# Kernel optimization log

Measured on AMD Instinct MI355X. Metric: run time of the kernel, lower is better.

## Reference

```python
import jax, jax.numpy as jnp
import numpy as np

B, CDD, HIS, S, D, NH, FF, V, K = 8, 5, 50, 64, 768, 12, 3072, 30522, 8


def _ln(x):
    mu = x.mean(-1, keepdims=True)
    var = ((x - mu) ** 2).mean(-1, keepdims=True)
    return (x - mu) / jnp.sqrt(var + 1e-12)


def _transformer(x, mask, Wq, Wk, Wv, Wo, W1, W2):
    # x: [..., S, D]; mask: [..., S] (float, >0 means valid)
    lead = x.shape[:-2]
    s, d = x.shape[-2], x.shape[-1]
    dh = d // NH
    x2 = x.reshape(-1, s, d)
    m = mask.reshape(-1, s)
    split = lambda t: t.reshape(-1, s, NH, dh).transpose(0, 2, 1, 3)
    q, k, v = split(x2 @ Wq), split(x2 @ Wk), split(x2 @ Wv)
    logits = jnp.einsum('nhqd,nhkd->nhqk', q, k) / jnp.sqrt(jnp.float32(dh))
    logits = logits + jnp.where(m > 0, 0.0, -1e9)[:, None, None, :]
    a = jax.nn.softmax(logits, axis=-1)
    o = jnp.einsum('nhqk,nhkd->nhqd', a, v).transpose(0, 2, 1, 3).reshape(-1, s, d) @ Wo
    h = _ln(x2 + o)
    h = _ln(h + jax.nn.gelu(h @ W1) @ W2)
    h = h.reshape(*lead, s, d)
    return h, h[..., 0, :]


def _build_prefix(subword_index, mask):
    # subword_index: [B, n, S, 2] int; mask: [B, n, 1] float
    b, n = subword_index.shape[0], subword_index.shape[1]
    flat = subword_index[..., 0] * S + subword_index[..., 1]  # [B, n, S]
    dest = jnp.zeros((b * n, S * S), jnp.float32)
    dest = dest.at[jnp.arange(b * n)[:, None], flat.reshape(b * n, S)].set(1.0)
    dest = dest * mask.reshape(b * n, 1)
    prefix = dest.reshape(b, n, S, S)
    # granularity == 'avg' -> L1 normalize rows
    prefix = prefix / jnp.maximum(prefix.sum(-1, keepdims=True), 1e-12)
    return prefix


def setup_inputs() -> dict:
    key = jax.random.key(0)
    ks = jax.random.split(key, 24)
    w = lambda k, shp: jax.random.normal(k, shp, jnp.float32) * 0.02
    inp = {
        'cdd_subword_index': jax.random.randint(ks[0], (B, CDD, S, 2), 0, S, jnp.int32),
        'his_subword_index': jax.random.randint(ks[1], (B, HIS, S, 2), 0, S, jnp.int32),
        'cdd_encoded_index': jax.random.randint(ks[2], (B, CDD, S), 0, V, jnp.int32),
        'his_encoded_index': jax.random.randint(ks[3], (B, HIS, S), 0, V, jnp.int32),
        'cdd_mask': jnp.ones((B, CDD, 1), jnp.float32),
        'his_mask': jnp.ones((B, HIS, 1), jnp.float32),
        'cdd_attn_mask': jnp.ones((B, CDD, S), jnp.float32),
        'his_attn_mask': jnp.ones((B, HIS, S), jnp.float32),
        'emb': w(ks[4], (V, D)),
        'bert_Wq': w(ks[5], (D, D)), 'bert_Wk': w(ks[6], (D, D)),
        'bert_Wv': w(ks[7], (D, D)), 'bert_Wo': w(ks[8], (D, D)),
        'bert_W1': w(ks[9], (D, FF)), 'bert_W2': w(ks[10], (FF, D)),
        'encN_Wq': w(ks[11], (D, D)), 'encN_Wk': w(ks[12], (D, D)),
        'encN_Wv': w(ks[13], (D, D)), 'encN_Wo': w(ks[14], (D, D)),
        'encN_W1': w(ks[15], (D, FF)), 'encN_W2': w(ks[16], (FF, D)),
        'qU': w(ks[17], (D,)),
        'proj_W': w(ks[18], (D, D)), 'proj_b': jnp.zeros((D,), jnp.float32),
    }
    return inp


def reference(cdd_subword_index, his_subword_index, cdd_encoded_index, his_encoded_index,
              cdd_mask, his_mask, cdd_attn_mask, his_attn_mask, emb,
              bert_Wq, bert_Wk, bert_Wv, bert_Wo, bert_W1, bert_W2,
              encN_Wq, encN_Wk, encN_Wv, encN_Wo, encN_W1, encN_W2,
              qU, proj_W, proj_b):
    rt_d = jnp.sqrt(jnp.float32(D))
    # scatter-built one-hot subword->token prefix matrices
    cdd_prefix = _build_prefix(cdd_subword_index, cdd_mask)   # [B,C,S,S]
    his_prefix = _build_prefix(his_subword_index, his_mask)   # [B,H,S,S]
    # pooled attention masks: prefix @ mask
    cdd_attn = jnp.einsum('bcst,bct->bcs', cdd_prefix, cdd_attn_mask)
    his_attn = jnp.einsum('bnst,bnt->bns', his_prefix, his_attn_mask)
    # embedding lookup + subword->token pooling
    cdd_emb = jnp.einsum('bcst,bctd->bcsd', cdd_prefix, emb[cdd_encoded_index])
    his_emb = jnp.einsum('bnst,bntd->bnsd', his_prefix, emb[his_encoded_index])
    # candidate news: BERT encode, take CLS, project
    _, cdd_cls = _transformer(cdd_emb, cdd_attn, bert_Wq, bert_Wk, bert_Wv, bert_Wo, bert_W1, bert_W2)
    cdd_repr = jnp.tanh(cdd_cls @ proj_W + proj_b)            # [B,C,D]
    # history news encoder
    his_hidden, his_cls = _transformer(his_emb, his_attn, encN_Wq, encN_Wk, encN_Wv, encN_Wo, encN_W1, encN_W2)
    # user encoder: attention pooling over history news reprs
    wgt = jax.nn.softmax(jnp.einsum('bnd,d->bn', his_cls, qU) / rt_d, axis=-1)
    user0 = jnp.einsum('bn,bnd->bd', wgt, his_cls)            # [B,D]
    # matching reducer: top-k personalized terms per history news
    scores = jnp.einsum('bnsd,bd->bns', his_hidden, user0) / rt_d
    scores = jnp.where(his_attn > 0, scores, -1e9)
    _, kid = jax.lax.top_k(scores, K)                         # [B,H,K]
    ps_terms = jnp.take_along_axis(his_hidden, kid[..., None], axis=2).reshape(B, HIS * K, D)
    ps_mask = jnp.take_along_axis(his_attn, kid, axis=2).reshape(B, HIS * K)
    # user BERT over selected terms
    _, user_cls = _transformer(ps_terms, ps_mask, bert_Wq, bert_Wk, bert_Wv, bert_Wo, bert_W1, bert_W2)
    user_repr = jnp.tanh(user_cls @ proj_W + proj_b)          # [B,D]
    score = jnp.einsum('bcd,bd->bc', cdd_repr, user_repr) / rt_d
    prob = jax.nn.log_softmax(score, axis=1)
    return prob, kid
```

## Files before the change

kernel.cpp:

```cpp
#include <hip/hip_runtime.h>
#include <math.h>

#define DIM 768
#define NHEAD 12
#define DHEAD 64
#define FFDIM 3072

typedef _Float16 v8h __attribute__((ext_vector_type(8)));
typedef float v4f __attribute__((ext_vector_type(4)));

__device__ __forceinline__ float gelu_f(float x) {
    float x3 = x * x * x;
    return 0.5f * x * (1.0f + tanhf(0.7978845608028654f * (x + 0.044715f * x3)));
}

__device__ __forceinline__ void gl_lds16(const _Float16* g, _Float16* l) {
    __builtin_amdgcn_global_load_lds(
        (const __attribute__((address_space(1))) unsigned int*)(g),
        (__attribute__((address_space(3))) unsigned int*)(l),
        16, 0, 0);
}

struct GemmP {
    const _Float16* A1; const _Float16* A2;
    const _Float16* eB1[3]; const _Float16* eB2[3]; const _Float16* bB1[3];
    float* C[3];
    _Float16* G1; _Float16* G2;
    int bnd;
};

__global__ __launch_bounds__(256) void gemm_mfma(GemmP p, int M, int N, int K,
                                                 int epi, float cdiv, float gscale, int nbg)
{
    __shared__ _Float16 sm[2][4][128 * 32];
    const int tid = threadIdx.x;
    const int w = tid >> 6, lane = tid & 63;
    const int lm = lane & 15, kg = lane >> 4;

    const int nb = (int)gridDim.x, mb = (int)gridDim.y;
    const int nwg = nb * mb * (int)gridDim.z;
    int lid = (int)blockIdx.x + nb * ((int)blockIdx.y + mb * (int)blockIdx.z);
    int qd = nwg >> 3, rm = nwg & 7;
    int xcd = lid & 7, pos = lid >> 3;
    int wid = (xcd < rm ? xcd * (qd + 1) : rm * (qd + 1) + (xcd - rm) * qd) + pos;
    int gsz = (nbg > 0 && (nb % nbg) == 0) ? nbg : 1;
    int ngrp = nb / gsz;
    int bxi = wid % gsz; int tt = wid / gsz;
    int by = tt % mb; tt /= mb;
    int bxg = tt % ngrp;
    int z = tt / ngrp;
    const int row0 = by << 7, col0 = (bxg * gsz + bxi) << 7;

    const int wm = (w >> 1) << 6, wn = (w & 1) << 6;
    const int rl = (w << 4) + (lane >> 2);
    const int cofs = (lane & 3) << 3;
    int nt; const _Float16 *B1p, *B2p;
    if (row0 < p.bnd) { nt = 3; B1p = p.eB1[z]; B2p = p.eB2[z]; }
    else             { nt = 1; B1p = p.bB1[z]; B2p = p.bB1[z]; }
    const _Float16* A1 = p.A1 + (size_t)row0 * K;
    const _Float16* A2 = p.A2 + (size_t)row0 * K;
    const _Float16* B1 = B1p + (size_t)col0 * K;
    const _Float16* B2 = B2p + (size_t)col0 * K;
    const int ldsLo = w * 512, ldsHi = (w + 4) * 512;
    const size_t gbase = (size_t)rl * K + cofs;

    v4f acc[4][4];
#pragma unroll
    for (int i = 0; i < 4; i++)
#pragma unroll
        for (int j = 0; j < 4; j++) acc[i][j] = (v4f){0.f, 0.f, 0.f, 0.f};

    auto stage = [&](int d, int k0) {
        size_t glo = gbase + k0;
        size_t ghi = glo + (size_t)64 * K;
        gl_lds16(A1 + glo, sm[d][0] + ldsLo); gl_lds16(A1 + ghi, sm[d][0] + ldsHi);
        gl_lds16(B1 + glo, sm[d][2] + ldsLo); gl_lds16(B1 + ghi, sm[d][2] + ldsHi);
        if (nt == 3) {
            gl_lds16(A2 + glo, sm[d][1] + ldsLo); gl_lds16(A2 + ghi, sm[d][1] + ldsHi);
            gl_lds16(B2 + glo, sm[d][3] + ldsLo); gl_lds16(B2 + ghi, sm[d][3] + ldsHi);
        }
    };

    const int nk = K >> 5;
    stage(0, 0);
    __syncthreads();
    for (int i = 0; i < nk; i++) {
        int cur = i & 1;
        if (i + 1 < nk) stage(cur ^ 1, (i + 1) << 5);
        const _Float16* sA1 = sm[cur][0]; const _Float16* sA2 = sm[cur][1];
        const _Float16* sB1 = sm[cur][2]; const _Float16* sB2 = sm[cur][3];
        v8h a1[4], b1f[4];
#pragma unroll
        for (int i2 = 0; i2 < 4; i2++) {
            a1[i2]  = *(const v8h*)(sA1 + (wm + (i2 << 4) + lm) * 32 + (kg << 3));
            b1f[i2] = *(const v8h*)(sB1 + (wn + (i2 << 4) + lm) * 32 + (kg << 3));
        }
        if (nt == 3) {
            v8h a2[4], b2f[4];
#pragma unroll
            for (int i2 = 0; i2 < 4; i2++) {
                a2[i2]  = *(const v8h*)(sA2 + (wm + (i2 << 4) + lm) * 32 + (kg << 3));
                b2f[i2] = *(const v8h*)(sB2 + (wn + (i2 << 4) + lm) * 32 + (kg << 3));
            }
#pragma unroll
            for (int i2 = 0; i2 < 4; i2++)
#pragma unroll
                for (int j = 0; j < 4; j++) {
                    acc[i2][j] = __builtin_amdgcn_mfma_f32_16x16x32_f16(a1[i2], b1f[j], acc[i2][j], 0, 0, 0);
                    acc[i2][j] = __builtin_amdgcn_mfma_f32_16x16x32_f16(a1[i2], b2f[j], acc[i2][j], 0, 0, 0);
                    acc[i2][j] = __builtin_amdgcn_mfma_f32_16x16x32_f16(a2[i2], b1f[j], acc[i2][j], 0, 0, 0);
                }
        } else {
#pragma unroll
            for (int i2 = 0; i2 < 4; i2++)
#pragma unroll
                for (int j = 0; j < 4; j++)
                    acc[i2][j] = __builtin_amdgcn_mfma_f32_16x16x32_f16(a1[i2], b1f[j], acc[i2][j], 0, 0, 0);
        }
        __syncthreads();
    }
    float* C = p.C[z];
#pragma unroll
    for (int i = 0; i < 4; i++) {
        int rb = row0 + wm + (i << 4) + (kg << 2);
#pragma unroll
        for (int j = 0; j < 4; j++) {
            int cc = col0 + wn + (j << 4) + lm;
#pragma unroll
            for (int r = 0; r < 4; r++) {
                float c = acc[i][j][r] * cdiv;
                size_t idx = (size_t)(rb + r) * N + cc;
                if (epi == 0) {
                    C[idx] = c;
                } else {
                    float gv = gelu_f(c) * gscale;
                    _Float16 g1 = (_Float16)gv;
                    p.G1[idx] = g1;
                    p.G2[idx] = (_Float16)(gv - (float)g1);
                }
            }
        }
    }
}

struct WJobs {
    const float* src[12];
    _Float16* d1[12]; _Float16* d2[12];
    int K[12]; int N[12]; int start[12];
};
__global__ __launch_bounds__(256) void wsplit_tr(WJobs jb)
{
    __shared__ float sh[32 * 33];
    int bid = blockIdx.x;
    int ji = 0;
#pragma unroll
    for (int i = 1; i < 12; i++) if (bid >= jb.start[i]) ji = i;
    const float* src = jb.src[ji];
    _Float16* d1 = jb.d1[ji]; _Float16* d2 = jb.d2[ji];
    int K = jb.K[ji], N = jb.N[ji];
    int t = bid - jb.start[ji];
    int tilesN = N >> 5;
    int tk = t / tilesN, tn = t - tk * tilesN;
    int k0 = tk << 5, n0 = tn << 5;
    int c = threadIdx.x & 31, rr = threadIdx.x >> 5;
#pragma unroll
    for (int pph = 0; pph < 4; pph++) {
        int r = rr + (pph << 3);
        sh[c * 33 + r] = src[(size_t)(k0 + r) * N + n0 + c];
    }
    __syncthreads();
#pragma unroll
    for (int pph = 0; pph < 4; pph++) {
        int rn = rr + (pph << 3);
        float v = sh[rn * 33 + c] * 64.f;
        _Float16 b1 = (_Float16)v;
        size_t idx = (size_t)(n0 + rn) * K + k0 + c;
        d1[idx] = b1;
        if (d2) d2[idx] = (_Float16)(v - (float)b1);
    }
}

__global__ __launch_bounds__(256) void build_prefix2(const int* __restrict__ hisSub,
    const float* __restrict__ hisMask, const float* __restrict__ hisAmask,
    const int* __restrict__ cddSub, const float* __restrict__ cddMask,
    const float* __restrict__ cddAmask,
    float* __restrict__ P, float* __restrict__ hisA, float* __restrict__ cddA)
{
    __shared__ float pref[64 * 64];
    int g = blockIdx.x;
    const int* sub; const float* mask; const float* amask; float* aout; int li;
    if (g < 400) { sub = hisSub; mask = hisMask; amask = hisAmask; aout = hisA; li = g; }
    else         { sub = cddSub; mask = cddMask; amask = cddAmask; aout = cddA; li = g - 400; }
    int tid = threadIdx.x;
    for (int t = tid; t < 4096; t += 256) pref[t] = 0.f;
    __syncthreads();
    if (tid < 64) {
        int r = sub[((size_t)li * 64 + tid) * 2 + 0];
        int c = sub[((size_t)li * 64 + tid) * 2 + 1];
        pref[(r << 6) + c] = 1.0f;
    }
    __syncthreads();
    float m = mask[li];
    int lane = tid & 63, w = tid >> 6;
    for (int s = (w << 4); s < (w << 4) + 16; s++) {
        float v = pref[(s << 6) + lane] * m;
        float rs = v;
#pragma unroll
        for (int o = 32; o; o >>= 1) rs += __shfl_down(rs, o);
        rs = __shfl(rs, 0);
        float nv = v / fmaxf(rs, 1e-12f);
        P[(((size_t)g << 6) + s) * 64 + lane] = nv;
        float av = nv * amask[((size_t)li << 6) + lane];
#pragma unroll
        for (int o = 32; o; o >>= 1) av += __shfl_down(av, o);
        if (lane == 0) aout[((size_t)li << 6) + s] = av;
    }
}

__global__ __launch_bounds__(256) void emb_pool2(const float* __restrict__ P,
    const int* __restrict__ encHis, const int* __restrict__ encCdd,
    const float* __restrict__ emb, float* __restrict__ X,
    _Float16* __restrict__ s1, _Float16* __restrict__ s2, int gOffHis, int gMid)
{
    int gl = blockIdx.x >> 2, q = blockIdx.x & 3;
    int g; const int* enc;
    if (gl < gMid) { g = gOffHis + gl; enc = encHis + (size_t)g * 64; }
    else { int gc = gl - gMid; g = 400 + gc; enc = encCdd + (size_t)gc * 64; }
    int tid = threadIdx.x;
    __shared__ float pw[16][64];
    __shared__ int tk[64];
    if (tid < 64) tk[tid] = enc[tid];
    for (int u = tid; u < 1024; u += 256) {
        int si = u >> 6, t = u & 63;
        pw[si][t] = P[((size_t)g * 64 + q * 16 + si) * 64 + t];
    }
    __syncthreads();
    float acc[16][3];
#pragma unroll
    for (int si = 0; si < 16; si++) { acc[si][0] = 0.f; acc[si][1] = 0.f; acc[si][2] = 0.f; }
    for (int t = 0; t < 64; t++) {
        const float* er = emb + (size_t)tk[t] * DIM;
        float e0 = er[tid], e1 = er[tid + 256], e2 = er[tid + 512];
#pragma unroll
        for (int si = 0; si < 16; si++) {
            float w = pw[si][t];
            acc[si][0] = fmaf(w, e0, acc[si][0]);
            acc[si][1] = fmaf(w, e1, acc[si][1]);
            acc[si][2] = fmaf(w, e2, acc[si][2]);
        }
    }
#pragma unroll
    for (int si = 0; si < 16; si++) {
        size_t base = ((size_t)gl * 64 + q * 16 + si) * DIM;
#pragma unroll
        for (int cci = 0; cci < 3; cci++) {
            int cc = tid + (cci << 8);
            float v = acc[si][cci];
            X[base + cc] = v;
            float xs = v * 64.f;
            _Float16 a = (_Float16)xs;
            s1[base + cc] = a;
            s2[base + cc] = (_Float16)(xs - (float)a);
        }
    }
}

__global__ __launch_bounds__(256) void attn_fused64(const float* __restrict__ Q,
    const float* __restrict__ Km, const float* __restrict__ V,
    const float* __restrict__ maskHis, const float* __restrict__ maskCdd, int gMid,
    _Float16* __restrict__ o1, _Float16* __restrict__ o2)
{
    __shared__ float Ks[64 * 65];
    __shared__ float Vs[64 * 65];
    __shared__ float Qs[64 * 65];
    int h = blockIdx.x % NHEAD;
    int g = blockIdx.x / NHEAD;
    const float* mrow = (g < gMid) ? maskHis + (size_t)g * 64
                                   : maskCdd + (size_t)(g - gMid) * 64;
    int tid = threadIdx.x, lane = tid & 63, w = tid >> 6;
    {
        int r = tid >> 2, c0 = (tid & 3) << 4;
        const float* qp = Q  + ((size_t)g * 64 + r) * DIM + h * DHEAD + c0;
        const float* kp = Km + ((size_t)g * 64 + r) * DIM + h * DHEAD + c0;
        const float* vp = V  + ((size_t)g * 64 + r) * DIM + h * DHEAD + c0;
#pragma unroll
        for (int u = 0; u < 16; u += 4) {
            float4 qv = *(const float4*)(qp + u);
            float4 kv = *(const float4*)(kp + u);
            float4 vv = *(const float4*)(vp + u);
            int o = r * 65 + c0 + u;
            Qs[o+0]=qv.x; Qs[o+1]=qv.y; Qs[o+2]=qv.z; Qs[o+3]=qv.w;
            Ks[o+0]=kv.x; Ks[o+1]=kv.y; Ks[o+2]=kv.z; Ks[o+3]=kv.w;
            Vs[o+0]=vv.x; Vs[o+1]=vv.y; Vs[o+2]=vv.z; Vs[o+3]=vv.w;
        }
    }
    __syncthreads();
    float mk = mrow[lane] > 0.f ? 0.f : -1e9f;
    for (int il = 0; il < 16; il++) {
        int i = (w << 4) + il;
        float d = 0.f;
        for (int t = 0; t < 64; t++) d = fmaf(Qs[i * 65 + t], Ks[lane * 65 + t], d);
        float l = d * 0.125f + mk;
        float mx = l;
#pragma unroll
        for (int o = 32; o; o >>= 1) mx = fmaxf(mx, __shfl_xor(mx, o));
        float e = expf(l - mx);
        float s = e;
#pragma unroll
        for (int o = 32; o; o >>= 1) s += __shfl_xor(s, o);
        float p = e / s;
        float acc = 0.f;
        for (int j = 0; j < 64; j++) {
            float pj = __shfl(p, j);
            acc = fmaf(pj, Vs[j * 65 + lane], acc);
        }
        size_t ob = ((size_t)g * 64 + i) * DIM + h * DHEAD + lane;
        float os = acc * 64.f;
        _Float16 h1 = (_Float16)os;
        o1[ob] = h1;
        o2[ob] = (_Float16)(os - (float)h1);
    }
}

#define SSTR 449
__global__ __launch_bounds__(256) void attn_flash400(const float* __restrict__ Q,
    const float* __restrict__ Km, const float* __restrict__ V,
    const float* __restrict__ mask, _Float16* __restrict__ o1, _Float16* __restrict__ o2)
{
    __shared__ _Float16 Kt[64 * 64];
    __shared__ float Sc[16 * SSTR];
    int qt = blockIdx.x % 25;
    int h  = (blockIdx.x / 25) % NHEAD;
    int g  = blockIdx.x / (25 * NHEAD);
    int tid = threadIdx.x, w = tid >> 6, lane = tid & 63, lm = lane & 15, kg = lane >> 4;

    v8h aq0, aq1;
    {
        const float* qp = Q + ((size_t)(g * 400 + qt * 16 + lm)) * DIM + h * DHEAD;
#pragma unroll
        for (int u = 0; u < 8; u++) {
            aq0[u] = (_Float16)qp[kg * 8 + u];
            aq1[u] = (_Float16)qp[32 + kg * 8 + u];
        }
    }
    for (int jt = 0; jt < 7; jt++) {
        int j0 = jt * 64;
        __syncthreads();
        {
            int jr = tid >> 2, c0 = (tid & 3) << 4;
            int j = j0 + jr;
            _Float16* kd = Kt + jr * 64 + c0;
            if (j < 400) {
                const float* kp = Km + ((size_t)(g * 400 + j)) * DIM + h * DHEAD + c0;
#pragma unroll
                for (int u = 0; u < 16; u++) kd[u] = (_Float16)kp[u];
            } else {
#pragma unroll
                for (int u = 0; u < 16; u++) kd[u] = (_Float16)0.f;
            }
        }
        __syncthreads();
        v8h b0, b1;
#pragma unroll
        for (int u = 0; u < 8; u++) {
            b0[u] = Kt[(w * 16 + lm) * 64 + kg * 8 + u];
            b1[u] = Kt[(w * 16 + lm) * 64 + 32 + kg * 8 + u];
        }
        v4f c = {0.f, 0.f, 0.f, 0.f};
        c = __builtin_amdgcn_mfma_f32_16x16x32_f16(aq0, b0, c, 0, 0, 0);
        c = __builtin_amdgcn_mfma_f32_16x16x32_f16(aq1, b1, c, 0, 0, 0);
        int jj = j0 + w * 16 + lm;
        float mv = (jj < 400) ? (mask[g * 400 + jj] > 0.f ? 0.f : -1e9f) : -1e9f;
#pragma unroll
        for (int r = 0; r < 4; r++)
            Sc[(kg * 4 + r) * SSTR + jj] = c[r] * 0.125f + mv;
    }
    __syncthreads();
    for (int rr = 0; rr < 4; rr++) {
        int r = w * 4 + rr;
        float mx = -INFINITY;
#pragma unroll
        for (int c7 = 0; c7 < 7; c7++) mx = fmaxf(mx, Sc[r * SSTR + c7 * 64 + lane]);
#pragma unroll
        for (int o = 32; o; o >>= 1) mx = fmaxf(mx, __shfl_xor(mx, o));
        float s = 0.f;
        float ev[7];
#pragma unroll
        for (int c7 = 0; c7 < 7; c7++) { ev[c7] = expf(Sc[r * SSTR + c7 * 64 + lane] - mx); s += ev[c7]; }
#pragma unroll
        for (int o = 32; o; o >>= 1) s += __shfl_xor(s, o);
        float inv = 1.f / s;
#pragma unroll
        for (int c7 = 0; c7 < 7; c7++) Sc[r * SSTR + c7 * 64 + lane] = ev[c7] * inv;
    }
    __syncthreads();
    v4f o = {0.f, 0.f, 0.f, 0.f};
    for (int kc = 0; kc < 14; kc++) {
        v8h a, b;
#pragma unroll
        for (int u = 0; u < 8; u++) a[u] = (_Float16)Sc[lm * SSTR + kc * 32 + kg * 8 + u];
#pragma unroll
        for (int u = 0; u < 8; u++) {
            int j = kc * 32 + kg * 8 + u;
            b[u] = (j < 400) ? (_Float16)V[((size_t)(g * 400 + j)) * DIM + h * DHEAD + w * 16 + lm]
                             : (_Float16)0.f;
        }
        o = __builtin_amdgcn_mfma_f32_16x16x32_f16(a, b, o, 0, 0, 0);
    }
#pragma unroll
    for (int r = 0; r < 4; r++) {
        int qr = qt * 16 + kg * 4 + r;
        size_t ob = ((size_t)(g * 400 + qr)) * DIM + h * DHEAD + w * 16 + lm;
        float os = o[r] * 64.f;
        _Float16 h1 = (_Float16)os;
        o1[ob] = h1; o2[ob] = (_Float16)(os - (float)h1);
    }
}

__global__ __launch_bounds__(256) void add_ln2(const float* __restrict__ X,
    const float* __restrict__ Y, float* __restrict__ outA, float* __restrict__ outB,
    int bndRow, _Float16* __restrict__ S1, _Float16* __restrict__ S2, float ss,
    float* __restrict__ cls, int clsOffA, int clsOffB, int S)
{
    int r = blockIdx.x, tid = threadIdx.x;
    size_t base = (size_t)r * DIM;
    float v0 = X[base + tid] + Y[base + tid];
    float v1 = X[base + tid + 256] + Y[base + tid + 256];
    float v2 = X[base + tid + 512] + Y[base + tid + 512];
    __shared__ float red[256];
    red[tid] = v0 + v1 + v2; __syncthreads();
    for (int o = 128; o; o >>= 1) { if (tid < o) red[tid] += red[tid + o]; __syncthreads(); }
    float mu = red[0] * (1.f / 768.f);
    __syncthreads();
    float d0 = v0 - mu, d1 = v1 - mu, d2 = v2 - mu;
    red[tid] = d0 * d0 + d1 * d1 + d2 * d2; __syncthreads();
    for (int o = 128; o; o >>= 1) { if (tid < o) red[tid] += red[tid + o]; __syncthreads(); }
    float rstd = rsqrtf(red[0] * (1.f / 768.f) + 1e-12f);
    float o0 = d0 * rstd, o1 = d1 * rstd, o2 = d2 * rstd;
    float* Out = (r < bndRow) ? outA + base : outB + (size_t)(r - bndRow) * DIM;
    Out[tid] = o0; Out[tid + 256] = o1; Out[tid + 512] = o2;
    if (S1) {
        float x0 = o0 * ss, x1 = o1 * ss, x2 = o2 * ss;
        _Float16 a0 = (_Float16)x0, a1 = (_Float16)x1, a2 = (_Float16)x2;
        S1[base + tid] = a0;        S2[base + tid] = (_Float16)(x0 - (float)a0);
        S1[base + tid + 256] = a1;  S2[base + tid + 256] = (_Float16)(x1 - (float)a1);
        S1[base + tid + 512] = a2;  S2[base + tid + 512] = (_Float16)(x2 - (float)a2);
    }
    if (cls && (r % S) == 0) {
        int g = (r < bndRow) ? clsOffA + r / S : clsOffB + (r - bndRow) / S;
        float* cd = cls + (size_t)g * DIM;
        cd[tid] = o0; cd[tid + 256] = o1; cd[tid + 512] = o2;
    }
}

__global__ __launch_bounds__(256) void gemm_kernel(const float* __restrict__ A,
    const float* __restrict__ B, float* __restrict__ C,
    int M, int N, int Kd, int epi, const float* __restrict__ bias)
{
    __shared__ float As[16][64];
    __shared__ float Bs[16][64];
    int tid = threadIdx.x;
    int tx = tid & 15, ty = tid >> 4;
    int row0 = blockIdx.y << 6, col0 = blockIdx.x << 6;
    int ar = tid >> 2, ak = (tid & 3) << 2;
    int bc = tid & 63, bk0 = tid >> 6;
    const float* Ap = A + (size_t)(row0 + ar) * Kd + ak;
    const float* Bp = B + (size_t)bk0 * N + col0 + bc;
    bool aval = (row0 + ar) < M;
    float acc[4][4];
#pragma unroll
    for (int i = 0; i < 4; i++)
#pragma unroll
        for (int j = 0; j < 4; j++) acc[i][j] = 0.f;
    for (int k0 = 0; k0 < Kd; k0 += 16) {
        float4 a4 = make_float4(0.f, 0.f, 0.f, 0.f);
        if (aval) a4 = *(const float4*)(Ap + k0);
        As[ak + 0][ar] = a4.x; As[ak + 1][ar] = a4.y;
        As[ak + 2][ar] = a4.z; As[ak + 3][ar] = a4.w;
#pragma unroll
        for (int i = 0; i < 4; i++)
            Bs[bk0 + 4 * i][bc] = Bp[(size_t)(k0 + 4 * i) * N];
        __syncthreads();
#pragma unroll
        for (int kk = 0; kk < 16; kk++) {
            float4 av = *(const float4*)&As[kk][ty << 2];
            float4 bv = *(const float4*)&Bs[kk][tx << 2];
            float aa[4] = {av.x, av.y, av.z, av.w};
            float bb[4] = {bv.x, bv.y, bv.z, bv.w};
#pragma unroll
            for (int i = 0; i < 4; i++)
#pragma unroll
                for (int j = 0; j < 4; j++)
                    acc[i][j] = fmaf(aa[i], bb[j], acc[i][j]);
        }
        __syncthreads();
    }
#pragma unroll
    for (int i = 0; i < 4; i++) {
        int r = row0 + (ty << 2) + i;
        if (r >= M) continue;
        float v[4];
#pragma unroll
        for (int j = 0; j < 4; j++) {
            float x = acc[i][j];
            if (epi == 1) x = gelu_f(x);
            else if (epi == 2) x = tanhf(x + bias[col0 + (tx << 2) + j]);
            v[j] = x;
        }
        *(float4*)(C + (size_t)r * N + col0 + (tx << 2)) = make_float4(v[0], v[1], v[2], v[3]);
    }
}

__global__ __launch_bounds__(256) void user_pool_kernel(const float* __restrict__ cls,
    const float* __restrict__ qU, float* __restrict__ user0)
{
    int b = blockIdx.x, tid = threadIdx.x;
    __shared__ float red[256];
    __shared__ float wv[64];
    const float scale = 0.03608439182435161f;
    for (int n = 0; n < 50; n++) {
        const float* cr = cls + ((size_t)(b * 50 + n)) * DIM;
        float d = 0.f;
        for (int t = tid; t < DIM; t += 256) d = fmaf(cr[t], qU[t], d);
        red[tid] = d; __syncthreads();
        for (int o = 128; o; o >>= 1) { if (tid < o) red[tid] += red[tid + o]; __syncthreads(); }
        if (tid == 0) wv[n] = red[0] * scale;
        __syncthreads();
    }
    if (tid == 0) {
        float mx = -INFINITY;
        for (int n = 0; n < 50; n++) mx = fmaxf(mx, wv[n]);
        float s = 0.f;
        for (int n = 0; n < 50; n++) { float e = expf(wv[n] - mx); wv[n] = e; s += e; }
        float inv = 1.f / s;
        for (int n = 0; n < 50; n++) wv[n] *= inv;
    }
    __syncthreads();
    for (int d = tid; d < DIM; d += 256) {
        float a = 0.f;
        for (int n = 0; n < 50; n++) a = fmaf(wv[n], cls[((size_t)(b * 50 + n)) * DIM + d], a);
        user0[(size_t)b * DIM + d] = a;
    }
}

__global__ __launch_bounds__(256) void topk_kernel(const float* __restrict__ hid,
    const float* __restrict__ user0, const float* __restrict__ attn,
    float* __restrict__ kid_f, int* __restrict__ kid_i, float* __restrict__ ps_mask)
{
    int bn = blockIdx.x;
    int b = bn / 50;
    int tid = threadIdx.x, lane = tid & 63, w = tid >> 6;
    __shared__ float sc[64];
    const float* u = user0 + (size_t)b * DIM;
    const float scale = 0.03608439182435161f;
    for (int s = w; s < 64; s += 4) {
        const float* hr = hid + ((size_t)bn * 64 + s) * DIM;
        float d = 0.f;
        for (int t = lane; t < DIM; t += 64) d = fmaf(hr[t], u[t], d);
#pragma unroll
        for (int o = 32; o; o >>= 1) d += __shfl_down(d, o);
        if (lane == 0) {
            float a = attn[(size_t)bn * 64 + s];
            sc[s] = (a > 0.f) ? d * scale : -1e9f;
        }
    }
    __syncthreads();
    if (tid == 0) {
        unsigned long long used = 0ull;
        for (int k = 0; k < 8; k++) {
            float best = -INFINITY; int bi = 0;
            for (int s = 0; s < 64; s++) {
                if ((used >> s) & 1ull) continue;
                if (sc[s] > best) { best = sc[s]; bi = s; }
            }
            used |= (1ull << bi);
            kid_i[bn * 8 + k] = bi;
            kid_f[bn * 8 + k] = (float)bi;
            ps_mask[bn * 8 + k] = attn[(size_t)bn * 64 + bi];
        }
    }
}

__global__ void gather2(const float* __restrict__ hid, const int* __restrict__ kid_i,
    float* __restrict__ X, _Float16* __restrict__ s1, _Float16* __restrict__ s2)
{
    int r = blockIdx.x, tid = threadIdx.x;
    int s = kid_i[r];
    int bn = r >> 3;
    const float* src = hid + ((size_t)bn * 64 + s) * DIM;
    size_t base = (size_t)r * DIM;
#pragma unroll
    for (int cci = 0; cci < 3; cci++) {
        int cc = tid + (cci << 8);
        float v = src[cc];
        X[base + cc] = v;
        float xs = v * 64.f;
        _Float16 a = (_Float16)xs;
        s1[base + cc] = a;
        s2[base + cc] = (_Float16)(xs - (float)a);
    }
}

__global__ __launch_bounds__(256) void final_kernel(const float* __restrict__ cdd_repr,
    const float* __restrict__ user_repr, float* __restrict__ out)
{
    int b = blockIdx.x, tid = threadIdx.x;
    __shared__ float red[256];
    __shared__ float sc[5];
    const float scale = 0.03608439182435161f;
    for (int c = 0; c < 5; c++) {
        const float* cr = cdd_repr + ((size_t)(b * 5 + c)) * DIM;
        const float* ur = user_repr + (size_t)b * DIM;
        float d = 0.f;
        for (int t = tid; t < DIM; t += 256) d = fmaf(cr[t], ur[t], d);
        red[tid] = d; __syncthreads();
        for (int o = 128; o; o >>= 1) { if (tid < o) red[tid] += red[tid + o]; __syncthreads(); }
        if (tid == 0) sc[c] = red[0] * scale;
        __syncthreads();
    }
    if (tid == 0) {
        float mx = -INFINITY;
        for (int c = 0; c < 5; c++) mx = fmaxf(mx, sc[c]);
        float s = 0.f;
        for (int c = 0; c < 5; c++) s += expf(sc[c] - mx);
        float lse = logf(s) + mx;
        for (int c = 0; c < 5; c++) out[b * 5 + c] = sc[c] - lse;
    }
}

extern "C" void kernel_launch(void* const* d_in, const int* in_sizes, int n_in,
                              void* d_out, int out_size, void* d_ws, size_t ws_size,
                              hipStream_t stream)
{
    (void)in_sizes; (void)n_in; (void)out_size;
    const int*   cdd_sub   = (const int*)d_in[0];
    const int*   his_sub   = (const int*)d_in[1];
    const int*   cdd_enc   = (const int*)d_in[2];
    const int*   his_enc   = (const int*)d_in[3];
    const float* cdd_mask  = (const float*)d_in[4];
    const float* his_mask  = (const float*)d_in[5];
    const float* cdd_amask = (const float*)d_in[6];
    const float* his_amask = (const float*)d_in[7];
    const float* emb = (const float*)d_in[8];
    const float* bWsrc[6] = {(const float*)d_in[9],  (const float*)d_in[10], (const float*)d_in[11],
                             (const float*)d_in[12], (const float*)d_in[13], (const float*)d_in[14]};
    const float* eWsrc[6] = {(const float*)d_in[15], (const float*)d_in[16], (const float*)d_in[17],
                             (const float*)d_in[18], (const float*)d_in[19], (const float*)d_in[20]};
    const float* qU = (const float*)d_in[21];
    const float* pW = (const float*)d_in[22];
    const float* pb = (const float*)d_in[23];
    float* out = (float*)d_out;

    auto al256 = [](size_t b) { return (b + 255) & ~(size_t)255; };
    auto needBytes = [&](size_t RCx) -> size_t {
        size_t t = 0;
        t += 4 * al256(RCx * 768 * 4);
        t += 2 * al256(RCx * 768 * 2);
        t += al256(RCx * 3072 * 2);
        t += al256((size_t)440 * 4096 * 4);
        t += al256((size_t)400 * 64 * 768 * 4);
        t += al256((size_t)448 * 768 * 4);
        t += 8 * al256(131072);
        t += 3 * (4 * al256((size_t)589824 * 2) + 2 * al256((size_t)2359296 * 2));
        return t;
    };
    const int NSopts[9] = {400, 200, 134, 100, 66, 50, 34, 24, 10};
    int NS = 10;
    for (int i = 0; i < 9; i++) {
        size_t RCt = (size_t)NSopts[i] * 64 + 2560;
        if (needBytes(RCt) <= ws_size) { NS = NSopts[i]; break; }
    }
    const size_t RC = (size_t)NS * 64 + 2560;

    char* wsb = (char*)d_ws;
    size_t off = 0;
    auto allocB = [&](size_t bytes) { char* p = wsb + off; off += al256(bytes); return p; };
    float* R_X = (float*)allocB(RC * 768 * 4);
    float* R_Q = (float*)allocB(RC * 768 * 4);
    float* R_K = (float*)allocB(RC * 768 * 4);
    float* R_V = (float*)allocB(RC * 768 * 4);
    _Float16* s1h = (_Float16*)allocB(RC * 768 * 2);
    _Float16* s2h = (_Float16*)allocB(RC * 768 * 2);
    _Float16* g2h = (_Float16*)allocB(RC * 3072 * 2);
    float* Pa   = (float*)allocB((size_t)440 * 4096 * 4);
    float* hisH = (float*)allocB((size_t)400 * 64 * 768 * 4);
    float* cls  = (float*)allocB((size_t)448 * 768 * 4);
    float* userC = (float*)allocB(131072);
    float* hisA  = (float*)allocB(131072);
    float* cddA  = (float*)allocB(131072);
    float* cddR  = (float*)allocB(131072);
    float* userR = (float*)allocB(131072);
    float* user0 = (float*)allocB(131072);
    float* psM   = (float*)allocB(131072);
    int*   kidI  = (int*)allocB(131072);
    size_t wsz[6] = {589824, 589824, 589824, 589824, 2359296, 2359296};
    _Float16 *eB1s[6], *eB2s[6], *bB1s[6];
    for (int i = 0; i < 6; i++) eB1s[i] = (_Float16*)allocB(wsz[i] * 2);
    for (int i = 0; i < 6; i++) eB2s[i] = (_Float16*)allocB(wsz[i] * 2);
    for (int i = 0; i < 6; i++) bB1s[i] = (_Float16*)allocB(wsz[i] * 2);
    _Float16* g1h = (_Float16*)R_K;
    float* cddTrash = (float*)g2h;

    int wk[6] = {768, 768, 768, 768, 768, 3072};
    int wn[6] = {768, 768, 768, 768, 3072, 768};
    {
        WJobs jb{};
        int st = 0;
        for (int i = 0; i < 6; i++) {
            jb.src[i] = eWsrc[i]; jb.d1[i] = eB1s[i]; jb.d2[i] = eB2s[i];
            jb.K[i] = wk[i]; jb.N[i] = wn[i]; jb.start[i] = st;
            st += (wk[i] >> 5) * (wn[i] >> 5);
        }
        for (int i = 0; i < 6; i++) {
            jb.src[6 + i] = bWsrc[i]; jb.d1[6 + i] = bB1s[i]; jb.d2[6 + i] = nullptr;
            jb.K[6 + i] = wk[i]; jb.N[6 + i] = wn[i]; jb.start[6 + i] = st;
            st += (wk[i] >> 5) * (wn[i] >> 5);
        }
        wsplit_tr<<<st, 256, 0, stream>>>(jb);
    }

    build_prefix2<<<440, 256, 0, stream>>>(his_sub, his_mask, his_amask,
                                           cdd_sub, cdd_mask, cdd_amask, Pa, hisA, cddA);

    auto mkP = [&](int sl, int bnd) {
        GemmP g{};
        g.A1 = s1h; g.A2 = s2h;
        for (int z = 0; z < 3; z++) {
            g.eB1[z] = eB1s[sl]; g.eB2[z] = eB2s[sl]; g.bB1[z] = bB1s[sl];
        }
        g.bnd = bnd;
        return g;
    };

    auto tf = [&](int M, int bnd, int nseqTot, int gMid, const float* mHis,
                  float* outA, float* outB, float* clsArena, int clsOffA, int clsOffB,
                  int S, bool userAttn) {
        int MB = M >> 7;
        GemmP gq = mkP(0, bnd);
        for (int z = 0; z < 3; z++) { gq.eB1[z] = eB1s[z]; gq.eB2[z] = eB2s[z]; gq.bB1[z] = bB1s[z]; }
        gq.C[0] = R_Q; gq.C[1] = R_K; gq.C[2] = R_V;
        gemm_mfma<<<dim3(6, MB, 3), 256, 0, stream>>>(gq, M, 768, 768, 0, 1.f / 4096.f, 0.f, 6);
        if (!userAttn) {
            attn_fused64<<<nseqTot * NHEAD, 256, 0, stream>>>(R_Q, R_K, R_V, mHis, cddA, gMid, s1h, s2h);
        } else {
            attn_flash400<<<8 * NHEAD * 25, 256, 0, stream>>>(R_Q, R_K, R_V, mHis, s1h, s2h);
        }
        GemmP go = mkP(3, bnd);
        go.C[0] = R_Q;
        gemm_mfma<<<dim3(6, MB, 1), 256, 0, stream>>>(go, M, 768, 768, 0, 1.f / 4096.f, 0.f, 6);
        add_ln2<<<M, 256, 0, stream>>>(R_X, R_Q, R_X, R_X, M, s1h, s2h, 1.f, nullptr, 0, 0, 64);
        GemmP g1 = mkP(4, bnd);
        g1.G1 = g1h; g1.G2 = g2h;
        gemm_mfma<<<dim3(24, MB, 1), 256, 0, stream>>>(g1, M, 3072, 768, 1, 1.f / 64.f, 16.f, 6);
        GemmP g2 = mkP(5, bnd);
        g2.A1 = g1h; g2.A2 = g2h; g2.C[0] = R_Q;
        gemm_mfma<<<dim3(6, MB, 1), 256, 0, stream>>>(g2, M, 768, 3072, 0, 1.f / 1024.f, 0.f, 2);
        add_ln2<<<M, 256, 0, stream>>>(R_X, R_Q, outA, outB, bnd, nullptr, nullptr, 0.f,
                                       clsArena, clsOffA, clsOffB, S);
    };

    int done = 0;
    bool first = true;
    while (done < 400) {
        int ns = NS < (400 - done) ? NS : (400 - done);
        int hisRows = ns * 64;
        int M = hisRows + (first ? 2560 : 0);
        int nseqTot = ns + (first ? 40 : 0);
        emb_pool2<<<nseqTot * 4, 256, 0, stream>>>(Pa, his_enc, cdd_enc, emb, R_X, s1h, s2h, done, ns);
        tf(M, hisRows, nseqTot, ns, hisA + (size_t)done * 64,
           hisH + (size_t)done * 64 * DIM, cddTrash, cls, done, 400, 64, false);
        done += ns;
        first = false;
    }

    gemm_kernel<<<dim3(12, 1), 256, 0, stream>>>(cls + (size_t)400 * 768, pW, cddR, 40, 768, 768, 2, pb);

    user_pool_kernel<<<8, 256, 0, stream>>>(cls, qU, user0);
    topk_kernel<<<400, 256, 0, stream>>>(hisH, user0, hisA, out + 40, kidI, psM);
    gather2<<<3200, 256, 0, stream>>>(hisH, kidI, R_X, s1h, s2h);

    tf(3200, 0, 8, 0, psM, hisH, hisH, userC, 0, 0, 400, true);
    gemm_kernel<<<dim3(12, 1), 256, 0, stream>>>(userC, pW, userR, 8, 768, 768, 2, pb);

    final_kernel<<<8, 256, 0, stream>>>(cddR, userR, out);
}
```

Baseline: 3.160 ms.

## Swizzle GEMM LDS tiles and load B2 operand directly from global

Applies an XOR swizzle to the column chunks written to and read from LDS in the split-precision MFMA GEMM, so that fragment reads hit fewer bank conflicts. The B2 (low-part) weight operand is no longer staged through LDS; each lane loads it from global memory into registers at the start of each k-step. This shrinks shared memory from four tiles to three per buffer. The MFMA sequence is also reordered so the a1*b1 products run first and the a2 fragment loads are issued later. The trade-off is strided, less coalesced global loads for B2 on the critical path, in exchange for less LDS traffic and a smaller footprint that may allow higher occupancy.

```diff
diff --git a/kernel.cpp b/kernel.cpp
--- a/kernel.cpp
+++ b/kernel.cpp
@@ -32,7 +32,7 @@
 __global__ __launch_bounds__(256) void gemm_mfma(GemmP p, int M, int N, int K,
                                                  int epi, float cdiv, float gscale, int nbg)
 {
-    __shared__ _Float16 sm[2][4][128 * 32];
+    __shared__ _Float16 sm[2][3][128 * 32];
     const int tid = threadIdx.x;
     const int w = tid >> 6, lane = tid & 63;
     const int lm = lane & 15, kg = lane >> 4;
@@ -53,7 +53,8 @@
 
     const int wm = (w >> 1) << 6, wn = (w & 1) << 6;
     const int rl = (w << 4) + (lane >> 2);
-    const int cofs = (lane & 3) << 3;
+    const int cofs = (((lane & 3) ^ ((lane >> 3) & 3)) << 3);
+    const int ks = ((kg ^ ((lm >> 1) & 3)) << 3);
     int nt; const _Float16 *B1p, *B2p;
     if (row0 < p.bnd) { nt = 3; B1p = p.eB1[z]; B2p = p.eB2[z]; }
     else             { nt = 1; B1p = p.bB1[z]; B2p = p.bB1[z]; }
@@ -77,7 +78,6 @@
         gl_lds16(B1 + glo, sm[d][2] + ldsLo); gl_lds16(B1 + ghi, sm[d][2] + ldsHi);
         if (nt == 3) {
             gl_lds16(A2 + glo, sm[d][1] + ldsLo); gl_lds16(A2 + ghi, sm[d][1] + ldsHi);
-            gl_lds16(B2 + glo, sm[d][3] + ldsLo); gl_lds16(B2 + ghi, sm[d][3] + ldsHi);
         }
     };
 
@@ -86,36 +86,42 @@
     __syncthreads();
     for (int i = 0; i < nk; i++) {
         int cur = i & 1;
+        int k0 = i << 5;
+        v8h b2f[4];
+        if (nt == 3) {
+#pragma unroll
+            for (int j = 0; j < 4; j++)
+                b2f[j] = *(const v8h*)(B2 + (size_t)(wn + (j << 4) + lm) * K + k0 + (kg << 3));
+        }
         if (i + 1 < nk) stage(cur ^ 1, (i + 1) << 5);
         const _Float16* sA1 = sm[cur][0]; const _Float16* sA2 = sm[cur][1];
-        const _Float16* sB1 = sm[cur][2]; const _Float16* sB2 = sm[cur][3];
+        const _Float16* sB1 = sm[cur][2];
         v8h a1[4], b1f[4];
 #pragma unroll
         for (int i2 = 0; i2 < 4; i2++) {
-            a1[i2]  = *(const v8h*)(sA1 + (wm + (i2 << 4) + lm) * 32 + (kg << 3));
-            b1f[i2] = *(const v8h*)(sB1 + (wn + (i2 << 4) + lm) * 32 + (kg << 3));
-        }
+            a1[i2]  = *(const v8h*)(sA1 + (wm + (i2 << 4) + lm) * 32 + ks);
+            b1f[i2] = *(const v8h*)(sB1 + (wn + (i2 << 4) + lm) * 32 + ks);
+        }
+#pragma unroll
+        for (int i2 = 0; i2 < 4; i2++)
+#pragma unroll
+            for (int j = 0; j < 4; j++)
+                acc[i2][j] = __builtin_amdgcn_mfma_f32_16x16x32_f16(a1[i2], b1f[j], acc[i2][j], 0, 0, 0);
         if (nt == 3) {
-            v8h a2[4], b2f[4];
-#pragma unroll
-            for (int i2 = 0; i2 < 4; i2++) {
-                a2[i2]  = *(const v8h*)(sA2 + (wm + (i2 << 4) + lm) * 32 + (kg << 3));
-                b2f[i2] = *(const v8h*)(sB2 + (wn + (i2 << 4) + lm) * 32 + (kg << 3));
-            }
 #pragma unroll
             for (int i2 = 0; i2 < 4; i2++)
 #pragma unroll
-                for (int j = 0; j < 4; j++) {
-                    acc[i2][j] = __builtin_amdgcn_mfma_f32_16x16x32_f16(a1[i2], b1f[j], acc[i2][j], 0, 0, 0);
+                for (int j = 0; j < 4; j++)
                     acc[i2][j] = __builtin_amdgcn_mfma_f32_16x16x32_f16(a1[i2], b2f[j], acc[i2][j], 0, 0, 0);
+            v8h a2[4];
+#pragma unroll
+            for (int i2 = 0; i2 < 4; i2++)
+                a2[i2] = *(const v8h*)(sA2 + (wm + (i2 << 4) + lm) * 32 + ks);
+#pragma unroll
+            for (int i2 = 0; i2 < 4; i2++)
+#pragma unroll
+                for (int j = 0; j < 4; j++)
                     acc[i2][j] = __builtin_amdgcn_mfma_f32_16x16x32_f16(a2[i2], b1f[j], acc[i2][j], 0, 0, 0);
-                }
-        } else {
-#pragma unroll
-            for (int i2 = 0; i2 < 4; i2++)
-#pragma unroll
-                for (int j = 0; j < 4; j++)
-                    acc[i2][j] = __builtin_amdgcn_mfma_f32_16x16x32_f16(a1[i2], b1f[j], acc[i2][j], 0, 0, 0);
         }
         __syncthreads();
     }
```

New measurement: 3.362 ms. 1.06x slower.

## Fuse Q/K/V projections into one GEMM kernel sharing the A tile

Applied to the files above, without the earlier changes.

Adds a dedicated gemm_qkv kernel that computes the Q, K and V projections in one workgroup, loading each A tile (hi/lo fp16 split) into LDS once and reusing it against all three weight matrices. Previously a z-dimension of 3 launched separate workgroups that each reloaded A. The price is a 3x larger accumulator set (192 floats per lane) and 64KB of LDS with launch_bounds(256,1), which lowers occupancy and drops the double-buffered pipelining of the original kernel.

```diff
diff --git a/kernel.cpp b/kernel.cpp
--- a/kernel.cpp
+++ b/kernel.cpp
@@ -28,6 +28,128 @@
     _Float16* G1; _Float16* G2;
     int bnd;
 };
+
+__global__ __launch_bounds__(256, 1) void gemm_qkv(GemmP p, int N, int K, float cdiv)
+{
+    __shared__ _Float16 sm[8 * 4096];
+    const int tid = threadIdx.x;
+    const int w = tid >> 6, lane = tid & 63;
+    const int lm = lane & 15, kg = lane >> 4;
+
+    const int nb = (int)gridDim.x, mb = (int)gridDim.y;
+    const int nwg = nb * mb;
+    int lid = (int)blockIdx.x + nb * (int)blockIdx.y;
+    int qd = nwg >> 3, rm = nwg & 7;
+    int xcd = lid & 7, pos = lid >> 3;
+    int wid = (xcd < rm ? xcd * (qd + 1) : rm * (qd + 1) + (xcd - rm) * qd) + pos;
+    int bxi = wid % nb, by = wid / nb;
+    const int row0 = by << 7, col0 = bxi << 7;
+
+    const int wm = (w >> 1) << 6, wn = (w & 1) << 6;
+    const int rl = (w << 4) + (lane >> 2);
+    const int cofs = (lane & 3) << 3;
+    const int ksl = kg << 3;
+    const int nt = (row0 < p.bnd) ? 3 : 1;
+    const _Float16 *B1z0, *B1z1, *B1z2, *B2z0, *B2z1, *B2z2;
+    if (nt == 3) {
+        B1z0 = p.eB1[0] + (size_t)col0 * K; B2z0 = p.eB2[0] + (size_t)col0 * K;
+        B1z1 = p.eB1[1] + (size_t)col0 * K; B2z1 = p.eB2[1] + (size_t)col0 * K;
+        B1z2 = p.eB1[2] + (size_t)col0 * K; B2z2 = p.eB2[2] + (size_t)col0 * K;
+    } else {
+        B1z0 = p.bB1[0] + (size_t)col0 * K; B2z0 = B1z0;
+        B1z1 = p.bB1[1] + (size_t)col0 * K; B2z1 = B1z1;
+        B1z2 = p.bB1[2] + (size_t)col0 * K; B2z2 = B1z2;
+    }
+    const _Float16* A1 = p.A1 + (size_t)row0 * K;
+    const _Float16* A2 = p.A2 + (size_t)row0 * K;
+    const int ldsLo = w * 512, ldsHi = (w + 4) * 512;
+    const size_t gbase = (size_t)rl * K + cofs;
+
+    v4f acc0[4][4], acc1[4][4], acc2[4][4];
+#pragma unroll
+    for (int i = 0; i < 4; i++)
+#pragma unroll
+        for (int j = 0; j < 4; j++) {
+            acc0[i][j] = (v4f){0.f, 0.f, 0.f, 0.f};
+            acc1[i][j] = (v4f){0.f, 0.f, 0.f, 0.f};
+            acc2[i][j] = (v4f){0.f, 0.f, 0.f, 0.f};
+        }
+
+    const int nk = K >> 5;
+    for (int i = 0; i < nk; i++) {
+        __syncthreads();
+        size_t glo = gbase + (size_t)(i << 5);
+        size_t ghi = glo + (size_t)64 * K;
+        gl_lds16(A1 + glo,   sm + 0 * 4096 + ldsLo); gl_lds16(A1 + ghi,   sm + 0 * 4096 + ldsHi);
+        gl_lds16(B1z0 + glo, sm + 2 * 4096 + ldsLo); gl_lds16(B1z0 + ghi, sm + 2 * 4096 + ldsHi);
+        gl_lds16(B1z1 + glo, sm + 4 * 4096 + ldsLo); gl_lds16(B1z1 + ghi, sm + 4 * 4096 + ldsHi);
+        gl_lds16(B1z2 + glo, sm + 6 * 4096 + ldsLo); gl_lds16(B1z2 + ghi, sm + 6 * 4096 + ldsHi);
+        if (nt == 3) {
+            gl_lds16(A2 + glo,   sm + 1 * 4096 + ldsLo); gl_lds16(A2 + ghi,   sm + 1 * 4096 + ldsHi);
+            gl_lds16(B2z0 + glo, sm + 3 * 4096 + ldsLo); gl_lds16(B2z0 + ghi, sm + 3 * 4096 + ldsHi);
+            gl_lds16(B2z1 + glo, sm + 5 * 4096 + ldsLo); gl_lds16(B2z1 + ghi, sm + 5 * 4096 + ldsHi);
+            gl_lds16(B2z2 + glo, sm + 7 * 4096 + ldsLo); gl_lds16(B2z2 + ghi, sm + 7 * 4096 + ldsHi);
+        }
+        __syncthreads();
+        v8h a1[4], a2[4];
+#pragma unroll
+        for (int i2 = 0; i2 < 4; i2++)
+            a1[i2] = *(const v8h*)(sm + 0 * 4096 + (wm + (i2 << 4) + lm) * 32 + ksl);
+        if (nt == 3) {
+#pragma unroll
+            for (int i2 = 0; i2 < 4; i2++)
+                a2[i2] = *(const v8h*)(sm + 1 * 4096 + (wm + (i2 << 4) + lm) * 32 + ksl);
+        }
+        auto dotz = [&](int bt1, int bt2, v4f (&az)[4][4]) {
+            const _Float16* s1 = sm + bt1 * 4096;
+            v8h b1f[4];
+#pragma unroll
+            for (int j = 0; j < 4; j++)
+                b1f[j] = *(const v8h*)(s1 + (wn + (j << 4) + lm) * 32 + ksl);
+#pragma unroll
+            for (int i2 = 0; i2 < 4; i2++)
+#pragma unroll
+                for (int j = 0; j < 4; j++)
+                    az[i2][j] = __builtin_amdgcn_mfma_f32_16x16x32_f16(a1[i2], b1f[j], az[i2][j], 0, 0, 0);
+            if (nt == 3) {
+                const _Float16* s2 = sm + bt2 * 4096;
+                v8h b2f[4];
+#pragma unroll
+                for (int j = 0; j < 4; j++)
+                    b2f[j] = *(const v8h*)(s2 + (wn + (j << 4) + lm) * 32 + ksl);
+#pragma unroll
+                for (int i2 = 0; i2 < 4; i2++)
+#pragma unroll
+                    for (int j = 0; j < 4; j++)
+                        az[i2][j] = __builtin_amdgcn_mfma_f32_16x16x32_f16(a1[i2], b2f[j], az[i2][j], 0, 0, 0);
+#pragma unroll
+                for (int i2 = 0; i2 < 4; i2++)
+#pragma unroll
+                    for (int j = 0; j < 4; j++)
+                        az[i2][j] = __builtin_amdgcn_mfma_f32_16x16x32_f16(a2[i2], b1f[j], az[i2][j], 0, 0, 0);
+            }
+        };
+        dotz(2, 3, acc0);
+        dotz(4, 5, acc1);
+        dotz(6, 7, acc2);
+    }
+    auto wrC = [&](float* C, v4f (&az)[4][4]) {
+#pragma unroll
+        for (int i = 0; i < 4; i++) {
+            int rb = row0 + wm + (i << 4) + (kg << 2);
+#pragma unroll
+            for (int j = 0; j < 4; j++) {
+                int cc = col0 + wn + (j << 4) + lm;
+#pragma unroll
+                for (int r = 0; r < 4; r++)
+                    C[(size_t)(rb + r) * N + cc] = az[i][j][r] * cdiv;
+            }
+        }
+    };
+    wrC(p.C[0], acc0);
+    wrC(p.C[1], acc1);
+    wrC(p.C[2], acc2);
+}
 
 __global__ __launch_bounds__(256) void gemm_mfma(GemmP p, int M, int N, int K,
                                                  int epi, float cdiv, float gscale, int nbg)
@@ -739,7 +861,7 @@
         GemmP gq = mkP(0, bnd);
         for (int z = 0; z < 3; z++) { gq.eB1[z] = eB1s[z]; gq.eB2[z] = eB2s[z]; gq.bB1[z] = bB1s[z]; }
         gq.C[0] = R_Q; gq.C[1] = R_K; gq.C[2] = R_V;
-        gemm_mfma<<<dim3(6, MB, 3), 256, 0, stream>>>(gq, M, 768, 768, 0, 1.f / 4096.f, 0.f, 6);
+        gemm_qkv<<<dim3(6, MB), 256, 0, stream>>>(gq, 768, 768, 1.f / 4096.f);
         if (!userAttn) {
             attn_fused64<<<nseqTot * NHEAD, 256, 0, stream>>>(R_Q, R_K, R_V, mHis, cddA, gMid, s1h, s2h);
         } else {
```

Result: slower. 3.447 ms (+9.1%).
